# Kernel tuning notes

Measured on AMD Instinct MI355X. Metric: run time of the kernel, lower is better.

## Reference

```python
import jax, jax.numpy as jnp
from jax import lax
import numpy as np

# pywt sym4 analysis filters (pywt.Wavelet('sym4').dec_lo / .dec_hi)
DEC_LO = np.array([-0.07576571478927333, -0.02963552764599851, 0.49761866763201545,
                   0.8037387518059161, 0.29785779560527736, -0.09921954357684722,
                   -0.012603967262037833, 0.0322231006040427], dtype=np.float32)
DEC_HI = np.array([-0.0322231006040427, -0.012603967262037833, 0.09921954357684722,
                   0.29785779560527736, -0.8037387518059161, 0.49761866763201545,
                   0.02963552764599851, -0.07576571478927333], dtype=np.float32)
L = 8            # sym4 filter length
LEVEL = 4
THRESH = 10.0


def _conv1d(x, kernel, stride, pad):
    # x: (B, T), kernel: (L,) used in correlation sense by lax.conv
    y = lax.conv_general_dilated(x[:, None, :], kernel[None, None, :],
                                 window_strides=(stride,), padding=[pad],
                                 dimension_numbers=('NCH', 'OIH', 'NCH'))
    return y[:, 0, :]


def _dwt1(x, filt):
    # pywt single-level DWT, mode='symmetric':
    #   pad L-1 each side (half-sample symmetric), true convolution, take odd-index
    #   outputs of the 'valid' part -> length floor((N+L-1)/2)
    ext = jnp.pad(x, ((0, 0), (L - 1, L - 1)), mode='symmetric')[:, 1:]
    return _conv1d(ext, filt[::-1], 2, (0, 0))  # flip -> true convolution


def _idwt1(cA, cD, lo, hi):
    # pywt single-level IDWT: upsample by 2, full-convolve with rec filters, sum,
    # trim L-2 from the left, output length 2*n - L + 2.
    B, n = cA.shape
    upA = jnp.zeros((B, 2 * n), cA.dtype).at[:, ::2].set(cA)
    upD = jnp.zeros((B, 2 * n), cD.dtype).at[:, ::2].set(cD)
    # rec_lo = dec_lo[::-1]; full conv w/ rec_lo == correlation w/ dec_lo
    y = _conv1d(upA, lo, 1, (L - 1, L - 1)) + _conv1d(upD, hi, 1, (L - 1, L - 1))
    return y[:, L - 2: L - 2 + 2 * n - L + 2]


def _wavelet_denoise(x):
    lo = jnp.asarray(DEC_LO)
    hi = jnp.asarray(DEC_HI)
    a = x
    details = []
    for _ in range(LEVEL):
        details.append(_dwt1(a, hi))
        a = _dwt1(a, lo)
    # hard threshold: KEEP coefficients with |c| <= threshold, zero the rest
    details = [jnp.where(jnp.abs(d) <= THRESH, d, jnp.zeros_like(d)) for d in details]
    rec = a
    for d in reversed(details):
        if rec.shape[1] > d.shape[1]:     # pywt waverec a[:-1] trim
            rec = rec[:, :d.shape[1]]
        rec = _idwt1(rec, d, lo, hi)
    return rec


def setup_inputs() -> dict:
    key = jax.random.key(0)
    k1, k2 = jax.random.split(key)
    x = jax.random.normal(k1, (100000, 512), dtype=jnp.float32) * 20.0
    edge_index = jax.random.randint(k2, (2, 100000), 0, 100000, dtype=jnp.int64)
    return {"x": x, "edge_index": edge_index, "num_nodes": 100000}


def reference(x, edge_index, num_nodes):
    # edge_index / num_nodes are unused by the original forward
    return _wavelet_denoise(x)
```

## Files before the change

kernel.cpp:

```cpp
#include <hip/hip_runtime.h>
#include <cstddef>

typedef float f2 __attribute__((ext_vector_type(2)));
typedef float f4 __attribute__((ext_vector_type(4)));
typedef _Float16 h2 __attribute__((ext_vector_type(2)));

#define THRESH_V 10.0f
#define WPB 2
#define SLICE_F2 930

static __device__ __forceinline__ void wave_sync() {
  asm volatile("s_waitcnt lgkmcnt(0)" ::: "memory");
}

#define L0f (-0.07576571478927333f)
#define L1f (-0.02963552764599851f)
#define L2f ( 0.49761866763201545f)
#define L3f ( 0.8037387518059161f)
#define L4f ( 0.29785779560527736f)
#define L5f (-0.09921954357684722f)
#define L6f (-0.012603967262037833f)
#define L7f ( 0.0322231006040427f)
#define H0f (-0.0322231006040427f)
#define H1f (-0.012603967262037833f)
#define H2f ( 0.09921954357684722f)
#define H3f ( 0.29785779560527736f)
#define H4f (-0.8037387518059161f)
#define H5f ( 0.49761866763201545f)
#define H6f ( 0.02963552764599851f)
#define H7f (-0.07576571478927333f)

static __device__ __forceinline__ void fill_ext(f2* E, f2* O, int n, int lane) {
  int k = 0; bool act = false;
  if (lane < 6)                    { k = -1 - lane;      act = true; }
  else if (lane >= 8 && lane < 15) { k = n + (lane - 8); act = true; }
  if (act) {
    const int src = (k < 0) ? (-1 - k) : (2 * n - 1 - k);
    const f2 v = (src & 1) ? O[src >> 1] : E[src >> 1];
    if (k & 1) O[(k - 1) >> 1] = v;
    else       E[k >> 1] = v;
  }
}

template <bool SPLIT_OUT, bool D16>
static __device__ __forceinline__ void fwd_stage(const f2* __restrict__ E,
                                                 const f2* __restrict__ O, int n,
                                                 f2* __restrict__ caE,
                                                 f2* __restrict__ caO,
                                                 void* __restrict__ cdv, int lane) {
#pragma clang fp contract(off)
  const int m = (n + 7) >> 1;
  f2* const cdf = (f2*)cdv;
  h2* const cdh = (h2*)cdv;
  f2* const myCa = SPLIT_OUT ? ((lane & 1) ? caO : caE) : caE;
  for (int i = lane; i < m; i += 64) {
    const f2* e = E + i - 3;
    const f2* o = O + i - 3;
    f2 v0 = e[0], v2 = e[1], v4 = e[2], v6 = e[3];
    f2 v1 = o[0], v3 = o[1], v5 = o[2], v7 = o[3];
    f2 sLo = ((v0 * L7f + v1 * L6f) + (v2 * L5f + v3 * L4f)) +
             ((v4 * L3f + v5 * L2f) + (v6 * L1f + v7 * L0f));
    f2 sHi = ((v0 * H7f + v1 * H6f) + (v2 * H5f + v3 * H4f)) +
             ((v4 * H3f + v5 * H2f) + (v6 * H1f + v7 * H0f));
    if constexpr (SPLIT_OUT) myCa[i >> 1] = sLo;
    else                     caE[i] = sLo;
    const float dx = (fabsf(sHi.x) <= THRESH_V) ? sHi.x : 0.f;
    const float dy = (fabsf(sHi.y) <= THRESH_V) ? sHi.y : 0.f;
    if constexpr (D16) {
      h2 r; r.x = (_Float16)dx; r.y = (_Float16)dy;
      cdh[i] = r;
    } else {
      f2 d; d.x = dx; d.y = dy;
      cdf[i] = d;
    }
  }
}

template <bool D16, bool GOUT>
static __device__ __forceinline__ void inv_stage(const f2* __restrict__ ca,
                                                 const void* __restrict__ cdv,
                                                 f2* __restrict__ dst,
                                                 float* __restrict__ gA,
                                                 float* __restrict__ gB, bool hasB,
                                                 int outLen, int lane) {
#pragma clang fp contract(fast)
  const f2* const cf = (const f2*)cdv;
  const h2* const ch = (const h2*)cdv;
  const int pairs = (outLen + 1) >> 1;
  for (int t = lane; t < pairs; t += 64) {
    f2 a0 = ca[t], a1 = ca[t + 1], a2 = ca[t + 2], a3 = ca[t + 3];
    f2 e0, e1, e2, e3;
    if constexpr (D16) {
      h2 x0 = ch[t], x1 = ch[t + 1], x2 = ch[t + 2], x3 = ch[t + 3];
      e0.x = (float)x0.x; e0.y = (float)x0.y;
      e1.x = (float)x1.x; e1.y = (float)x1.y;
      e2.x = (float)x2.x; e2.y = (float)x2.y;
      e3.x = (float)x3.x; e3.y = (float)x3.y;
    } else {
      e0 = cf[t]; e1 = cf[t + 1]; e2 = cf[t + 2]; e3 = cf[t + 3];
    }
    f2 se = a0 * L1f + a1 * L3f + a2 * L5f + a3 * L7f +
            e0 * H1f + e1 * H3f + e2 * H5f + e3 * H7f;
    f2 so = a0 * L0f + a1 * L2f + a2 * L4f + a3 * L6f +
            e0 * H0f + e1 * H2f + e2 * H4f + e3 * H6f;
    const int q = 2 * t;
    if constexpr (GOUT) {
      *reinterpret_cast<float2*>(gA + q) = make_float2(se.x, so.x);
      if (hasB) *reinterpret_cast<float2*>(gB + q) = make_float2(se.y, so.y);
    } else {
      if (q + 1 < outLen) {
        f4 r; r.x = se.x; r.y = se.y; r.z = so.x; r.w = so.y;
        *reinterpret_cast<f4*>(dst + q) = r;
      } else {
        dst[q] = se;
      }
    }
  }
}

__global__ __launch_bounds__(128, 8) void wavelet_denoise_kernel(
    const float* __restrict__ x, float* __restrict__ out, int nrows) {
  __shared__ __align__(16) f2 lds[WPB][SLICE_F2];
  const int wave = threadIdx.x >> 6;
  const int lane = threadIdx.x & 63;
  const int nPairs = (nrows + 1) >> 1;
  const int pairId = blockIdx.x * WPB + wave;
  if (pairId >= nPairs) return;

  const int rA = 2 * pairId;
  const bool hasB = (rA + 1) < nrows;
  const int rBc = hasB ? rA + 1 : rA;

  f2* Sp   = lds[wave];
  f2* sxE  = Sp + 4;    f2* sxO  = Sp + 268;
  f2* ca1E = Sp + 531;  f2* ca1O = Sp + 667;
  h2* d1   = (h2*)(Sp + 800);
  f2* ca2E = Sp + 4;    f2* ca2O = Sp + 78;
  f2* d2   = Sp + 148;
  f2* ca3E = Sp + 286;  f2* ca3O = Sp + 328;
  f2* d3   = Sp + 366;
  f2* ca4  = Sp + 436;  f2* d4   = Sp + 474;
  f2* rec70  = Sp + 528;
  f2* rec133 = Sp + 0;
  f2* rec259 = Sp + 528;

  {
    const float4* sA4 = reinterpret_cast<const float4*>(x + (size_t)rA * 512);
    const float4* sB4 = reinterpret_cast<const float4*>(x + (size_t)rBc * 512);
    for (int c = lane; c < 128; c += 64) {
      float4 a = sA4[c];
      float4 b = sB4[c];
      f4 ev; ev.x = a.x; ev.y = b.x; ev.z = a.z; ev.w = b.z;
      f4 ov; ov.x = a.y; ov.y = b.y; ov.z = a.w; ov.w = b.w;
      *reinterpret_cast<f4*>(sxE + 2 * c) = ev;
      *reinterpret_cast<f4*>(sxO + 2 * c) = ov;
    }
  }
  wave_sync();
  fill_ext(sxE, sxO, 512, lane); wave_sync();

  fwd_stage<true,  true >(sxE,  sxO,  512, ca1E, ca1O, d1, lane); wave_sync();
  fill_ext(ca1E, ca1O, 259, lane);                                wave_sync();
  fwd_stage<true,  false>(ca1E, ca1O, 259, ca2E, ca2O, d2, lane); wave_sync();
  fill_ext(ca2E, ca2O, 133, lane);                                wave_sync();
  fwd_stage<true,  false>(ca2E, ca2O, 133, ca3E, ca3O, d3, lane); wave_sync();
  fill_ext(ca3E, ca3O, 70, lane);                                 wave_sync();
  fwd_stage<false, false>(ca3E, ca3O, 70, ca4, nullptr, d4, lane); wave_sync();

  float* gA = out + (size_t)rA * 512;
  float* gB = out + (size_t)rBc * 512;
  inv_stage<false, false>(ca4,    d4, rec70,  nullptr, nullptr, false,  70, lane);
  wave_sync();
  inv_stage<false, false>(rec70,  d3, rec133, nullptr, nullptr, false, 133, lane);
  wave_sync();
  inv_stage<false, false>(rec133, d2, rec259, nullptr, nullptr, false, 259, lane);
  wave_sync();
  inv_stage<true,  true >(rec259, d1, nullptr, gA, gB, hasB, 512, lane);
}

extern "C" void kernel_launch(void* const* d_in, const int* in_sizes, int n_in,
                              void* d_out, int out_size, void* d_ws, size_t ws_size,
                              hipStream_t stream) {
  const float* x = (const float*)d_in[0];
  float* out = (float*)d_out;
  const int nrows = in_sizes[0] / 512;
  const int nPairs = (nrows + 1) >> 1;
  const int grid = (nPairs + WPB - 1) / WPB;
  wavelet_denoise_kernel<<<dim3(grid), dim3(WPB * 64), 0, stream>>>(x, out, nrows);
}
```

Before: 343.0 us.

## Interleave LDS signal layout and fold symmetric padding into forward stages

Stores each level's signal contiguously instead of as separate even/odd arrays, so each forward output reads its 8 taps as four 16-byte LDS loads. The producing stage writes the symmetric boundary margins directly, which removes the separate fill_ext passes and their extra wave syncs. Stage lengths become template constants so the loops fully unroll. The launch-bounds occupancy hint is relaxed from 8 to 4, and the boundary writes add branches whose mirrored indices must be exactly right.

```diff
diff --git a/kernel.cpp b/kernel.cpp
--- a/kernel.cpp
+++ b/kernel.cpp
@@ -7,7 +7,7 @@
 
 #define THRESH_V 10.0f
 #define WPB 2
-#define SLICE_F2 930
+#define SLICE_F2 928
 
 static __device__ __forceinline__ void wave_sync() {
   asm volatile("s_waitcnt lgkmcnt(0)" ::: "memory");
@@ -30,95 +30,94 @@
 #define H6f ( 0.02963552764599851f)
 #define H7f (-0.07576571478927333f)
 
-static __device__ __forceinline__ void fill_ext(f2* E, f2* O, int n, int lane) {
-  int k = 0; bool act = false;
-  if (lane < 6)                    { k = -1 - lane;      act = true; }
-  else if (lane >= 8 && lane < 15) { k = n + (lane - 8); act = true; }
-  if (act) {
-    const int src = (k < 0) ? (-1 - k) : (2 * n - 1 - k);
-    const f2 v = (src & 1) ? O[src >> 1] : E[src >> 1];
-    if (k & 1) O[(k - 1) >> 1] = v;
-    else       E[k >> 1] = v;
-  }
-}
-
-template <bool SPLIT_OUT, bool D16>
-static __device__ __forceinline__ void fwd_stage(const f2* __restrict__ E,
-                                                 const f2* __restrict__ O, int n,
-                                                 f2* __restrict__ caE,
-                                                 f2* __restrict__ caO,
+static __device__ __forceinline__ f2 lo2(f4 w) { return __builtin_shufflevector(w, w, 0, 1); }
+static __device__ __forceinline__ f2 hi2(f4 w) { return __builtin_shufflevector(w, w, 2, 3); }
+
+template <int N, bool MARGINS, bool D16>
+static __device__ __forceinline__ void fwd_stage(const f2* __restrict__ in,
+                                                 f2* __restrict__ ca,
                                                  void* __restrict__ cdv, int lane) {
 #pragma clang fp contract(off)
-  const int m = (n + 7) >> 1;
+  constexpr int M = (N + 7) >> 1;
   f2* const cdf = (f2*)cdv;
   h2* const cdh = (h2*)cdv;
-  f2* const myCa = SPLIT_OUT ? ((lane & 1) ? caO : caE) : caE;
-  for (int i = lane; i < m; i += 64) {
-    const f2* e = E + i - 3;
-    const f2* o = O + i - 3;
-    f2 v0 = e[0], v2 = e[1], v4 = e[2], v6 = e[3];
-    f2 v1 = o[0], v3 = o[1], v5 = o[2], v7 = o[3];
-    f2 sLo = ((v0 * L7f + v1 * L6f) + (v2 * L5f + v3 * L4f)) +
-             ((v4 * L3f + v5 * L2f) + (v6 * L1f + v7 * L0f));
-    f2 sHi = ((v0 * H7f + v1 * H6f) + (v2 * H5f + v3 * H4f)) +
-             ((v4 * H3f + v5 * H2f) + (v6 * H1f + v7 * H0f));
-    if constexpr (SPLIT_OUT) myCa[i >> 1] = sLo;
-    else                     caE[i] = sLo;
-    const float dx = (fabsf(sHi.x) <= THRESH_V) ? sHi.x : 0.f;
-    const float dy = (fabsf(sHi.y) <= THRESH_V) ? sHi.y : 0.f;
-    if constexpr (D16) {
-      h2 r; r.x = (_Float16)dx; r.y = (_Float16)dy;
-      cdh[i] = r;
-    } else {
-      f2 d; d.x = dx; d.y = dy;
-      cdf[i] = d;
+#pragma unroll
+  for (int k = 0; k * 64 < M; ++k) {
+    const int i = lane + k * 64;
+    if (i < M) {
+      const f4* w = (const f4*)(in + 2 * i - 6);
+      const f4 w0 = w[0], w1 = w[1], w2 = w[2], w3 = w[3];
+      const f2 v0 = lo2(w0), v1 = hi2(w0), v2 = lo2(w1), v3 = hi2(w1);
+      const f2 v4 = lo2(w2), v5 = hi2(w2), v6 = lo2(w3), v7 = hi2(w3);
+      f2 sLo = ((v0 * L7f + v1 * L6f) + (v2 * L5f + v3 * L4f)) +
+               ((v4 * L3f + v5 * L2f) + (v6 * L1f + v7 * L0f));
+      f2 sHi = ((v0 * H7f + v1 * H6f) + (v2 * H5f + v3 * H4f)) +
+               ((v4 * H3f + v5 * H2f) + (v6 * H1f + v7 * H0f));
+      ca[i] = sLo;
+      if constexpr (MARGINS) {
+        if (i < 6)      ca[-1 - i]        = sLo;
+        if (i >= M - 7) ca[2 * M - 1 - i] = sLo;
+      }
+      const float dx = (fabsf(sHi.x) <= THRESH_V) ? sHi.x : 0.f;
+      const float dy = (fabsf(sHi.y) <= THRESH_V) ? sHi.y : 0.f;
+      if constexpr (D16) {
+        h2 r; r.x = (_Float16)dx; r.y = (_Float16)dy;
+        cdh[i] = r;
+      } else {
+        f2 d; d.x = dx; d.y = dy;
+        cdf[i] = d;
+      }
     }
   }
 }
 
-template <bool D16, bool GOUT>
+template <int OUTLEN, bool D16, bool GOUT>
 static __device__ __forceinline__ void inv_stage(const f2* __restrict__ ca,
                                                  const void* __restrict__ cdv,
                                                  f2* __restrict__ dst,
                                                  float* __restrict__ gA,
                                                  float* __restrict__ gB, bool hasB,
-                                                 int outLen, int lane) {
+                                                 int lane) {
 #pragma clang fp contract(fast)
   const f2* const cf = (const f2*)cdv;
   const h2* const ch = (const h2*)cdv;
-  const int pairs = (outLen + 1) >> 1;
-  for (int t = lane; t < pairs; t += 64) {
-    f2 a0 = ca[t], a1 = ca[t + 1], a2 = ca[t + 2], a3 = ca[t + 3];
-    f2 e0, e1, e2, e3;
-    if constexpr (D16) {
-      h2 x0 = ch[t], x1 = ch[t + 1], x2 = ch[t + 2], x3 = ch[t + 3];
-      e0.x = (float)x0.x; e0.y = (float)x0.y;
-      e1.x = (float)x1.x; e1.y = (float)x1.y;
-      e2.x = (float)x2.x; e2.y = (float)x2.y;
-      e3.x = (float)x3.x; e3.y = (float)x3.y;
-    } else {
-      e0 = cf[t]; e1 = cf[t + 1]; e2 = cf[t + 2]; e3 = cf[t + 3];
-    }
-    f2 se = a0 * L1f + a1 * L3f + a2 * L5f + a3 * L7f +
-            e0 * H1f + e1 * H3f + e2 * H5f + e3 * H7f;
-    f2 so = a0 * L0f + a1 * L2f + a2 * L4f + a3 * L6f +
-            e0 * H0f + e1 * H2f + e2 * H4f + e3 * H6f;
-    const int q = 2 * t;
-    if constexpr (GOUT) {
-      *reinterpret_cast<float2*>(gA + q) = make_float2(se.x, so.x);
-      if (hasB) *reinterpret_cast<float2*>(gB + q) = make_float2(se.y, so.y);
-    } else {
-      if (q + 1 < outLen) {
-        f4 r; r.x = se.x; r.y = se.y; r.z = so.x; r.w = so.y;
-        *reinterpret_cast<f4*>(dst + q) = r;
+  constexpr int PAIRS = (OUTLEN + 1) >> 1;
+#pragma unroll
+  for (int k = 0; k * 64 < PAIRS; ++k) {
+    const int t = lane + k * 64;
+    if (t < PAIRS) {
+      f2 a0 = ca[t], a1 = ca[t + 1], a2 = ca[t + 2], a3 = ca[t + 3];
+      f2 e0, e1, e2, e3;
+      if constexpr (D16) {
+        h2 x0 = ch[t], x1 = ch[t + 1], x2 = ch[t + 2], x3 = ch[t + 3];
+        e0.x = (float)x0.x; e0.y = (float)x0.y;
+        e1.x = (float)x1.x; e1.y = (float)x1.y;
+        e2.x = (float)x2.x; e2.y = (float)x2.y;
+        e3.x = (float)x3.x; e3.y = (float)x3.y;
       } else {
-        dst[q] = se;
+        e0 = cf[t]; e1 = cf[t + 1]; e2 = cf[t + 2]; e3 = cf[t + 3];
+      }
+      f2 se = a0 * L1f + a1 * L3f + a2 * L5f + a3 * L7f +
+              e0 * H1f + e1 * H3f + e2 * H5f + e3 * H7f;
+      f2 so = a0 * L0f + a1 * L2f + a2 * L4f + a3 * L6f +
+              e0 * H0f + e1 * H2f + e2 * H4f + e3 * H6f;
+      const int q = 2 * t;
+      if constexpr (GOUT) {
+        *reinterpret_cast<float2*>(gA + q) = make_float2(se.x, so.x);
+        if (hasB) *reinterpret_cast<float2*>(gB + q) = make_float2(se.y, so.y);
+      } else {
+        if (q + 1 < OUTLEN) {
+          f4 r; r.x = se.x; r.y = se.y; r.z = so.x; r.w = so.y;
+          *reinterpret_cast<f4*>(dst + q) = r;
+        } else {
+          dst[q] = se;
+        }
       }
     }
   }
 }
 
-__global__ __launch_bounds__(128, 8) void wavelet_denoise_kernel(
+__global__ __launch_bounds__(128, 4) void wavelet_denoise_kernel(
     const float* __restrict__ x, float* __restrict__ out, int nrows) {
   __shared__ __align__(16) f2 lds[WPB][SLICE_F2];
   const int wave = threadIdx.x >> 6;
@@ -131,51 +130,69 @@
   const bool hasB = (rA + 1) < nrows;
   const int rBc = hasB ? rA + 1 : rA;
 
-  f2* Sp   = lds[wave];
-  f2* sxE  = Sp + 4;    f2* sxO  = Sp + 268;
-  f2* ca1E = Sp + 531;  f2* ca1O = Sp + 667;
-  h2* d1   = (h2*)(Sp + 800);
-  f2* ca2E = Sp + 4;    f2* ca2O = Sp + 78;
-  f2* d2   = Sp + 148;
-  f2* ca3E = Sp + 286;  f2* ca3O = Sp + 328;
-  f2* d3   = Sp + 366;
-  f2* ca4  = Sp + 436;  f2* d4   = Sp + 474;
-  f2* rec70  = Sp + 528;
+  f2* Sp  = lds[wave];
+  f2* sx  = Sp + 6;
+  f2* ca2 = Sp + 6;    f2* d2 = Sp + 146;
+  f2* ca3 = Sp + 286;  f2* d3 = Sp + 364;
+  f2* ca4 = Sp + 434;  f2* d4 = Sp + 472;
+  f2* ca1 = Sp + 532;
+  h2* d1  = (h2*)(Sp + 798);
+  f2* rec70  = Sp + 526;
   f2* rec133 = Sp + 0;
-  f2* rec259 = Sp + 528;
+  f2* rec259 = Sp + 526;
 
   {
     const float4* sA4 = reinterpret_cast<const float4*>(x + (size_t)rA * 512);
     const float4* sB4 = reinterpret_cast<const float4*>(x + (size_t)rBc * 512);
-    for (int c = lane; c < 128; c += 64) {
-      float4 a = sA4[c];
-      float4 b = sB4[c];
-      f4 ev; ev.x = a.x; ev.y = b.x; ev.z = a.z; ev.w = b.z;
-      f4 ov; ov.x = a.y; ov.y = b.y; ov.z = a.w; ov.w = b.w;
-      *reinterpret_cast<f4*>(sxE + 2 * c) = ev;
-      *reinterpret_cast<f4*>(sxO + 2 * c) = ov;
+#pragma unroll
+    for (int kk = 0; kk < 2; ++kk) {
+      const int c = lane + kk * 64;
+      const float4 a = sA4[c];
+      const float4 b = sB4[c];
+      f4 u0; u0.x = a.x; u0.y = b.x; u0.z = a.y; u0.w = b.y;
+      f4 u1; u1.x = a.z; u1.y = b.z; u1.z = a.w; u1.w = b.w;
+      *reinterpret_cast<f4*>(sx + 4 * c)     = u0;
+      *reinterpret_cast<f4*>(sx + 4 * c + 2) = u1;
+      if (c == 0) {
+        f4 m0; m0.x = a.y; m0.y = b.y; m0.z = a.x; m0.w = b.x;
+        *reinterpret_cast<f4*>(sx - 2) = m0;
+        f4 m1; m1.x = a.w; m1.y = b.w; m1.z = a.z; m1.w = b.z;
+        *reinterpret_cast<f4*>(sx - 4) = m1;
+      }
+      if (c == 1) {
+        f4 m; m.x = a.y; m.y = b.y; m.z = a.x; m.w = b.x;
+        *reinterpret_cast<f4*>(sx - 6) = m;
+      }
+      if (c == 127) {
+        f4 m0; m0.x = a.w; m0.y = b.w; m0.z = a.z; m0.w = b.z;
+        *reinterpret_cast<f4*>(sx + 512) = m0;
+        f4 m1; m1.x = a.y; m1.y = b.y; m1.z = a.x; m1.w = b.x;
+        *reinterpret_cast<f4*>(sx + 514) = m1;
+      }
+      if (c == 126) {
+        f4 m0; m0.x = a.w; m0.y = b.w; m0.z = a.z; m0.w = b.z;
+        *reinterpret_cast<f4*>(sx + 516) = m0;
+        f2 m1; m1.x = a.y; m1.y = b.y;
+        sx[518] = m1;
+      }
     }
   }
   wave_sync();
-  fill_ext(sxE, sxO, 512, lane); wave_sync();
-
-  fwd_stage<true,  true >(sxE,  sxO,  512, ca1E, ca1O, d1, lane); wave_sync();
-  fill_ext(ca1E, ca1O, 259, lane);                                wave_sync();
-  fwd_stage<true,  false>(ca1E, ca1O, 259, ca2E, ca2O, d2, lane); wave_sync();
-  fill_ext(ca2E, ca2O, 133, lane);                                wave_sync();
-  fwd_stage<true,  false>(ca2E, ca2O, 133, ca3E, ca3O, d3, lane); wave_sync();
-  fill_ext(ca3E, ca3O, 70, lane);                                 wave_sync();
-  fwd_stage<false, false>(ca3E, ca3O, 70, ca4, nullptr, d4, lane); wave_sync();
+
+  fwd_stage<512, true,  true >(sx,  ca1, d1, lane); wave_sync();
+  fwd_stage<259, true,  false>(ca1, ca2, d2, lane); wave_sync();
+  fwd_stage<133, true,  false>(ca2, ca3, d3, lane); wave_sync();
+  fwd_stage< 70, false, false>(ca3, ca4, d4, lane); wave_sync();
 
   float* gA = out + (size_t)rA * 512;
   float* gB = out + (size_t)rBc * 512;
-  inv_stage<false, false>(ca4,    d4, rec70,  nullptr, nullptr, false,  70, lane);
-  wave_sync();
-  inv_stage<false, false>(rec70,  d3, rec133, nullptr, nullptr, false, 133, lane);
-  wave_sync();
-  inv_stage<false, false>(rec133, d2, rec259, nullptr, nullptr, false, 259, lane);
-  wave_sync();
-  inv_stage<true,  true >(rec259, d1, nullptr, gA, gB, hasB, 512, lane);
+  inv_stage< 70, false, false>(ca4,    d4, rec70,  nullptr, nullptr, false, lane);
+  wave_sync();
+  inv_stage<133, false, false>(rec70,  d3, rec133, nullptr, nullptr, false, lane);
+  wave_sync();
+  inv_stage<259, false, false>(rec133, d2, rec259, nullptr, nullptr, false, lane);
+  wave_sync();
+  inv_stage<512, true,  true >(rec259, d1, nullptr, gA, gB, hasB, lane);
 }
 
 extern "C" void kernel_launch(void* const* d_in, const int* in_sizes, int n_in,
```

Result: no change. 341.4 us (-0.5%).
